# Kernel tuning notes

Hardware: AMD Instinct MI355X
Metric: run time of the kernel (lower is better)

## Reference

```python
import jax, jax.numpy as jnp
import numpy as np

B, P, N, C = 4, 12, 1024, 64  # batch, past window, nodes, channels (in==hidden==out)


def setup_inputs() -> dict:
    key = jax.random.key(0)
    k1, k2, k3, k4, k5, k6 = jax.random.split(key, 6)
    x = jax.random.normal(k1, (B, P, N, C), dtype=jnp.float32)
    # float adjacency mask in {0,1}; force self-loops so no softmax row is empty
    A = jax.random.randint(k2, (B, P, N, N), 0, 2).astype(jnp.float32)
    A = A.at[..., jnp.arange(N), jnp.arange(N)].set(1.0)
    # learned params (nn.Linear stores weight as [out, in]; y = x @ W.T)
    W_emb = jax.random.normal(k3, (C, C), dtype=jnp.float32) / jnp.sqrt(jnp.float32(C))
    a1 = jax.random.normal(k4, (C,), dtype=jnp.float32)
    a2 = jax.random.normal(k5, (C,), dtype=jnp.float32)
    W_lin = jax.random.normal(k6, (C, C), dtype=jnp.float32) / jnp.sqrt(jnp.float32(C))
    return {"x": x, "A": A, "W_emb": W_emb, "a1": a1, "a2": a2, "W_lin": W_lin}


def reference(x, A, W_emb, a1, a2, W_lin):
    # x_emb = emb(x)  (bias-free linear)
    x_emb = jnp.einsum('bpnc,hc->bpnh', x, W_emb)            # [B,P,N,H]
    s1 = x_emb @ a1                                           # [B,P,N]
    s2 = x_emb @ a2                                           # [B,P,N]
    # additive GAT scores: a1_i + a2_j, broadcast instead of repeat
    z = jax.nn.leaky_relu(s1[..., :, None] + s2[..., None, :], 0.01)  # [B,P,N,N]
    z = jnp.where(A == 0.0, -jnp.inf, z)
    pi = jax.nn.softmax(z, axis=-1)                           # masked attention
    agg = jnp.einsum('bpij,bpjc->bpic', pi, x)                # weighted aggregation
    out = jax.nn.sigmoid(jnp.einsum('bpic,oc->bpio', agg, W_lin))
    return (out, A)
```

## Files before the change

kernel.cpp:

```cpp
#include <hip/hip_runtime.h>

typedef __attribute__((ext_vector_type(8))) __bf16 bf16x8;
typedef __attribute__((ext_vector_type(4))) float f32x4;

#define N_ 1024
#define C_ 64
#define BP_ 48

static __device__ __forceinline__ unsigned short f2bf(float f) {
    __bf16 b = (__bf16)f;
    return __builtin_bit_cast(unsigned short, b);
}
static __device__ __forceinline__ unsigned int pack2(float a, float b) {
    return (unsigned int)f2bf(a) | ((unsigned int)f2bf(b) << 16);
}

__global__ __launch_bounds__(256) void gat_pre(
    const float* __restrict__ x, const float* __restrict__ Wemb,
    const float* __restrict__ a1, const float* __restrict__ a2,
    float* __restrict__ s1g, float* __restrict__ s2g,
    unsigned short* __restrict__ xT, float* __restrict__ M2part)
{
    __shared__ float xs[64][65];
    __shared__ float vs[2][64];
    const int t = threadIdx.x, l = t & 63, w = t >> 6;
    const int j0 = blockIdx.x * 64;
    const int bp = blockIdx.y;

    if (w == 0) {
        float v1 = 0.f, v2 = 0.f;
        #pragma unroll 8
        for (int h = 0; h < 64; ++h) {
            float we = Wemb[h * 64 + l];
            v1 = fmaf(a1[h], we, v1);
            v2 = fmaf(a2[h], we, v2);
        }
        vs[0][l] = v1; vs[1][l] = v2;
    }
    const float* xb = x + ((size_t)bp * N_ + j0) * C_;
    #pragma unroll
    for (int it = 0; it < 16; ++it)
        xs[it * 4 + w][l] = xb[(it * 4 + w) * C_ + l];
    __syncthreads();

    const int jr = t >> 2, c0 = (t & 3) * 16;
    float p1 = 0.f, p2 = 0.f;
    #pragma unroll
    for (int k = 0; k < 16; ++k) {
        float xv = xs[jr][c0 + k];
        p1 = fmaf(xv, vs[0][c0 + k], p1);
        p2 = fmaf(xv, vs[1][c0 + k], p2);
    }
    p1 += __shfl_xor(p1, 1); p1 += __shfl_xor(p1, 2);
    p2 += __shfl_xor(p2, 1); p2 += __shfl_xor(p2, 2);
    if ((l & 3) == 0) {
        s1g[bp * N_ + j0 + jr] = p1;
        s2g[bp * N_ + j0 + jr] = p2;
    }
    float m = p2;
    m = fmaxf(m, __shfl_xor(m, 4));
    m = fmaxf(m, __shfl_xor(m, 8));
    m = fmaxf(m, __shfl_xor(m, 16));
    m = fmaxf(m, __shfl_xor(m, 32));
    if (l == 0) M2part[bp * 64 + blockIdx.x * 4 + w] = m;

    const int c = t >> 2, part = t & 3;
    unsigned int ow[8];
    #pragma unroll
    for (int k = 0; k < 16; k += 2) {
        unsigned int lo = f2bf(xs[part * 16 + k][c]);
        unsigned int hi = f2bf(xs[part * 16 + k + 1][c]);
        ow[k >> 1] = lo | (hi << 16);
    }
    uint4* dst = (uint4*)(xT + (size_t)bp * C_ * N_ + (size_t)c * N_ + j0 + part * 16);
    dst[0] = make_uint4(ow[0], ow[1], ow[2], ow[3]);
    dst[1] = make_uint4(ow[4], ow[5], ow[6], ow[7]);
}

__global__ __launch_bounds__(256, 4) void gat_fused(
    const float* __restrict__ Ag, float* __restrict__ outA,
    const unsigned short* __restrict__ xT,
    const float* __restrict__ s1g, const float* __restrict__ s2g,
    const float* __restrict__ M2part,
    const float* __restrict__ Wlin, float* __restrict__ out)
{
    __shared__ unsigned short Plds[4][16][72];
    __shared__ float s2lds[1024];
    __shared__ float lsLDS[4][16];

    const int t = threadIdx.x, l = t & 63, w = t >> 6;
    const int i15 = l & 15, q = l >> 4;
    const int lm = l & 15, g16 = l >> 4;
    const int bp = blockIdx.y;
    const int ibase = blockIdx.x * 64 + w * 16;

    *(f32x4*)&s2lds[4 * t] = *(const f32x4*)&s2g[bp * N_ + 4 * t];

    float m2v = M2part[bp * 64 + l];
    #pragma unroll
    for (int off = 32; off >= 1; off >>= 1)
        m2v = fmaxf(m2v, __shfl_xor(m2v, off));
    const float M2 = m2v;
    const float s1_l = s1g[bp * N_ + ibase + i15];

    float s1r[4], mvr[4];
    #pragma unroll
    for (int sr = 0; sr < 4; ++sr) {
        s1r[sr] = __shfl(s1_l, 4 * sr + g16);
        float zr = s1r[sr] + M2;
        mvr[sr] = fmaxf(zr, 0.01f * zr);
    }

    __syncthreads();

    const float* Arow = Ag + ((size_t)bp * N_ + ibase + g16) * N_ + 4 * lm;
    float* oArow = outA + ((size_t)bp * N_ + ibase + g16) * N_ + 4 * lm;
    const unsigned short* xTb = xT + (size_t)bp * C_ * N_;

    f32x4 acc[4] = {};
    float ls4[4] = {0.f, 0.f, 0.f, 0.f};

    f32x4 Aa0, Aa1, Aa2, Aa3, Ab0, Ab1, Ab2, Ab3;

#define LOADA(d0, d1, d2, d3, kk) do {                                        \
    const float* _p = Arow + (kk) * 64;                                       \
    d0 = *(const f32x4*)(_p);                                                 \
    d1 = *(const f32x4*)(_p + 4 * N_);                                        \
    d2 = *(const f32x4*)(_p + 8 * N_);                                        \
    d3 = *(const f32x4*)(_p + 12 * N_); } while (0)

#define DOSR(Av, sr, j0c) do {                                                \
    *(f32x4*)(oArow + (sr) * 4 * N_ + (j0c)) = Av;                            \
    float e0, e1, e2, e3;                                                     \
    { float zz = s1r[sr] + s2v[0]; zz = fmaxf(zz, 0.01f * zz);                \
      e0 = (Av[0] != 0.f) ? __expf(zz - mvr[sr]) : 0.f; }                     \
    { float zz = s1r[sr] + s2v[1]; zz = fmaxf(zz, 0.01f * zz);                \
      e1 = (Av[1] != 0.f) ? __expf(zz - mvr[sr]) : 0.f; }                     \
    { float zz = s1r[sr] + s2v[2]; zz = fmaxf(zz, 0.01f * zz);                \
      e2 = (Av[2] != 0.f) ? __expf(zz - mvr[sr]) : 0.f; }                     \
    { float zz = s1r[sr] + s2v[3]; zz = fmaxf(zz, 0.01f * zz);                \
      e3 = (Av[3] != 0.f) ? __expf(zz - mvr[sr]) : 0.f; }                     \
    ls4[sr] += (e0 + e1) + (e2 + e3);                                         \
    *(uint2*)&Plds[w][4 * (sr) + g16][4 * lm] =                               \
        make_uint2(pack2(e0, e1), pack2(e2, e3)); } while (0)

#define CONSUME(a0, a1, a2, a3, kk) do {                                      \
    const int j0c = (kk) * 64;                                                \
    const f32x4 s2v = *(const f32x4*)&s2lds[j0c + 4 * lm];                    \
    DOSR(a0, 0, j0c); DOSR(a1, 1, j0c); DOSR(a2, 2, j0c); DOSR(a3, 3, j0c);  \
    _Pragma("unroll")                                                         \
    for (int s = 0; s < 2; ++s) {                                             \
        bf16x8 af = *(const bf16x8*)&Plds[w][i15][s * 32 + q * 8];            \
        _Pragma("unroll")                                                     \
        for (int nt = 0; nt < 4; ++nt) {                                      \
            bf16x8 bfr = *(const bf16x8*)&xTb[(size_t)(nt * 16 + i15) * N_ +  \
                                              j0c + s * 32 + q * 8];          \
            acc[nt] = __builtin_amdgcn_mfma_f32_16x16x32_bf16(af, bfr,        \
                                                              acc[nt], 0, 0, 0); \
        }                                                                     \
    } } while (0)

    LOADA(Aa0, Aa1, Aa2, Aa3, 0);
    #pragma unroll 1
    for (int k = 0; k < 16; k += 2) {
        LOADA(Ab0, Ab1, Ab2, Ab3, k + 1);
        CONSUME(Aa0, Aa1, Aa2, Aa3, k);
        if (k + 2 < 16)
            LOADA(Aa0, Aa1, Aa2, Aa3, k + 2);
        CONSUME(Ab0, Ab1, Ab2, Ab3, k + 1);
    }
#undef LOADA
#undef DOSR
#undef CONSUME

    #pragma unroll
    for (int sr = 0; sr < 4; ++sr) {
        ls4[sr] += __shfl_xor(ls4[sr], 1);
        ls4[sr] += __shfl_xor(ls4[sr], 2);
        ls4[sr] += __shfl_xor(ls4[sr], 4);
        ls4[sr] += __shfl_xor(ls4[sr], 8);
    }
    if (lm == 0) {
        #pragma unroll
        for (int sr = 0; sr < 4; ++sr)
            lsLDS[w][4 * sr + g16] = ls4[sr];
    }
    const f32x4 lsq = *(const f32x4*)&lsLDS[w][4 * q];

    unsigned short* aggl = &Plds[w][0][0];
    #pragma unroll
    for (int nt = 0; nt < 4; ++nt)
        #pragma unroll
        for (int r = 0; r < 4; ++r)
            aggl[(q * 4 + r) * 72 + nt * 16 + i15] = f2bf(acc[nt][r] / lsq[r]);

    f32x4 d2[4] = {};
    #pragma unroll
    for (int s = 0; s < 2; ++s) {
        bf16x8 af = *(const bf16x8*)&aggl[i15 * 72 + s * 32 + q * 8];
        #pragma unroll
        for (int nt = 0; nt < 4; ++nt) {
            const float* wp = Wlin + (size_t)(nt * 16 + i15) * C_ + s * 32 + q * 8;
            f32x4 w0 = *(const f32x4*)wp;
            f32x4 w1 = *(const f32x4*)(wp + 4);
            bf16x8 bfr;
            #pragma unroll
            for (int jj = 0; jj < 4; ++jj) { bfr[jj] = (__bf16)w0[jj]; bfr[4 + jj] = (__bf16)w1[jj]; }
            d2[nt] = __builtin_amdgcn_mfma_f32_16x16x32_bf16(af, bfr, d2[nt], 0, 0, 0);
        }
    }
    float* orow = out + ((size_t)bp * N_ + ibase) * C_;
    #pragma unroll
    for (int nt = 0; nt < 4; ++nt)
        #pragma unroll
        for (int r = 0; r < 4; ++r)
            orow[(size_t)(q * 4 + r) * C_ + nt * 16 + i15] =
                1.f / (1.f + __expf(-d2[nt][r]));
}

extern "C" void kernel_launch(void* const* d_in, const int* in_sizes, int n_in,
                              void* d_out, int out_size, void* d_ws, size_t ws_size,
                              hipStream_t stream) {
    const float* x    = (const float*)d_in[0];
    const float* Ag   = (const float*)d_in[1];
    const float* Wemb = (const float*)d_in[2];
    const float* a1   = (const float*)d_in[3];
    const float* a2   = (const float*)d_in[4];
    const float* Wlin = (const float*)d_in[5];
    float* out  = (float*)d_out;
    float* outA = out + (size_t)BP_ * N_ * C_;

    float* s1g = (float*)d_ws;
    float* s2g = s1g + BP_ * N_;
    float* M2part = s2g + BP_ * N_;
    unsigned short* xT = (unsigned short*)(M2part + BP_ * 64);

    gat_pre<<<dim3(16, BP_), dim3(256), 0, stream>>>(x, Wemb, a1, a2,
                                                     s1g, s2g, xT, M2part);
    gat_fused<<<dim3(16, BP_), dim3(256), 0, stream>>>(Ag, outA, xT, s1g, s2g,
                                                       M2part, Wlin, out);
}
```

Baseline: 403.5 us.

## Split key dimension across wave pairs and double grid for more parallelism

Each block now covers 32 query rows instead of 64. Two waves share each 16-row group, and each of the two handles half of the 1024 key columns. The partial aggregation accumulators and row sums are combined through shared memory before the projection epilogue. The grid doubles to 32x48 blocks and launch bounds rise to 6 blocks per SM, aiming to expose more memory-level parallelism for streaming the large A tensor. In exchange it adds an extra LDS buffer, a block-wide barrier, and idle waves during the epilogue.

```diff
diff --git a/kernel.cpp b/kernel.cpp
--- a/kernel.cpp
+++ b/kernel.cpp
@@ -77,7 +77,7 @@
     dst[1] = make_uint4(ow[4], ow[5], ow[6], ow[7]);
 }
 
-__global__ __launch_bounds__(256, 4) void gat_fused(
+__global__ __launch_bounds__(256, 6) void gat_fused(
     const float* __restrict__ Ag, float* __restrict__ outA,
     const unsigned short* __restrict__ xT,
     const float* __restrict__ s1g, const float* __restrict__ s2g,
@@ -87,12 +87,15 @@
     __shared__ unsigned short Plds[4][16][72];
     __shared__ float s2lds[1024];
     __shared__ float lsLDS[4][16];
+    __shared__ float comb[2][16][68];
 
     const int t = threadIdx.x, l = t & 63, w = t >> 6;
     const int i15 = l & 15, q = l >> 4;
     const int lm = l & 15, g16 = l >> 4;
     const int bp = blockIdx.y;
-    const int ibase = blockIdx.x * 64 + w * 16;
+    const int rg = w >> 1, jh = w & 1;
+    const int ibase = blockIdx.x * 32 + rg * 16;
+    const int jbase = jh * 512;
 
     *(f32x4*)&s2lds[4 * t] = *(const f32x4*)&s2g[bp * N_ + 4 * t];
 
@@ -113,8 +116,8 @@
 
     __syncthreads();
 
-    const float* Arow = Ag + ((size_t)bp * N_ + ibase + g16) * N_ + 4 * lm;
-    float* oArow = outA + ((size_t)bp * N_ + ibase + g16) * N_ + 4 * lm;
+    const float* Arow = Ag + ((size_t)bp * N_ + ibase + g16) * N_ + jbase + 4 * lm;
+    float* oArow = outA + ((size_t)bp * N_ + ibase + g16) * N_ + jbase + 4 * lm;
     const unsigned short* xTb = xT + (size_t)bp * C_ * N_;
 
     f32x4 acc[4] = {};
@@ -129,8 +132,8 @@
     d2 = *(const f32x4*)(_p + 8 * N_);                                        \
     d3 = *(const f32x4*)(_p + 12 * N_); } while (0)
 
-#define DOSR(Av, sr, j0c) do {                                                \
-    *(f32x4*)(oArow + (sr) * 4 * N_ + (j0c)) = Av;                            \
+#define DOSR(Av, sr, jrel) do {                                               \
+    *(f32x4*)(oArow + (sr) * 4 * N_ + (jrel)) = Av;                           \
     float e0, e1, e2, e3;                                                     \
     { float zz = s1r[sr] + s2v[0]; zz = fmaxf(zz, 0.01f * zz);                \
       e0 = (Av[0] != 0.f) ? __expf(zz - mvr[sr]) : 0.f; }                     \
@@ -145,9 +148,10 @@
         make_uint2(pack2(e0, e1), pack2(e2, e3)); } while (0)
 
 #define CONSUME(a0, a1, a2, a3, kk) do {                                      \
-    const int j0c = (kk) * 64;                                                \
+    const int jrel = (kk) * 64;                                               \
+    const int j0c = jbase + jrel;                                             \
     const f32x4 s2v = *(const f32x4*)&s2lds[j0c + 4 * lm];                    \
-    DOSR(a0, 0, j0c); DOSR(a1, 1, j0c); DOSR(a2, 2, j0c); DOSR(a3, 3, j0c);  \
+    DOSR(a0, 0, jrel); DOSR(a1, 1, jrel); DOSR(a2, 2, jrel); DOSR(a3, 3, jrel); \
     _Pragma("unroll")                                                         \
     for (int s = 0; s < 2; ++s) {                                             \
         bf16x8 af = *(const bf16x8*)&Plds[w][i15][s * 32 + q * 8];            \
@@ -162,10 +166,10 @@
 
     LOADA(Aa0, Aa1, Aa2, Aa3, 0);
     #pragma unroll 1
-    for (int k = 0; k < 16; k += 2) {
+    for (int k = 0; k < 8; k += 2) {
         LOADA(Ab0, Ab1, Ab2, Ab3, k + 1);
         CONSUME(Aa0, Aa1, Aa2, Aa3, k);
-        if (k + 2 < 16)
+        if (k + 2 < 8)
             LOADA(Aa0, Aa1, Aa2, Aa3, k + 2);
         CONSUME(Ab0, Ab1, Ab2, Ab3, k + 1);
     }
@@ -185,7 +189,26 @@
         for (int sr = 0; sr < 4; ++sr)
             lsLDS[w][4 * sr + g16] = ls4[sr];
     }
-    const f32x4 lsq = *(const f32x4*)&lsLDS[w][4 * q];
+    if (jh == 1) {
+        #pragma unroll
+        for (int nt = 0; nt < 4; ++nt)
+            #pragma unroll
+            for (int r = 0; r < 4; ++r)
+                comb[rg][q * 4 + r][nt * 16 + i15] = acc[nt][r];
+    }
+    __syncthreads();
+    if (jh == 1) return;
+
+    #pragma unroll
+    for (int nt = 0; nt < 4; ++nt)
+        #pragma unroll
+        for (int r = 0; r < 4; ++r)
+            acc[nt][r] += comb[rg][q * 4 + r][nt * 16 + i15];
+    const f32x4 ls_a = *(const f32x4*)&lsLDS[w][4 * q];
+    const f32x4 ls_b = *(const f32x4*)&lsLDS[w + 1][4 * q];
+    f32x4 lsq;
+    #pragma unroll
+    for (int r = 0; r < 4; ++r) lsq[r] = ls_a[r] + ls_b[r];
 
     unsigned short* aggl = &Plds[w][0][0];
     #pragma unroll
@@ -237,6 +260,6 @@
 
     gat_pre<<<dim3(16, BP_), dim3(256), 0, stream>>>(x, Wemb, a1, a2,
                                                      s1g, s2g, xT, M2part);
-    gat_fused<<<dim3(16, BP_), dim3(256), 0, stream>>>(Ag, outA, xT, s1g, s2g,
+    gat_fused<<<dim3(32, BP_), dim3(256), 0, stream>>>(Ag, outA, xT, s1g, s2g,
                                                        M2part, Wlin, out);
 }
```

Measured after the change: 472.1 us. 1.17x slower.

## Prefetch xT MFMA operands into registers and use nontemporal A load/store

Applied to the files above, without the earlier changes.

The bf16 xT fragments for each 64-column chunk are now loaded into registers one chunk ahead, double-buffered alongside the A tile, so the MFMA B operands are no longer fetched from global memory right before use. A loads and outA stores become nontemporal to avoid polluting cache with the streamed adjacency. Occupancy is lowered to 3 waves-per-SIMD blocks to make room for the extra prefetch registers. The cost is more register pressure and less latency hiding through occupancy.

```diff
diff --git a/kernel.cpp b/kernel.cpp
--- a/kernel.cpp
+++ b/kernel.cpp
@@ -77,7 +77,7 @@
     dst[1] = make_uint4(ow[4], ow[5], ow[6], ow[7]);
 }
 
-__global__ __launch_bounds__(256, 4) void gat_fused(
+__global__ __launch_bounds__(256, 3) void gat_fused(
     const float* __restrict__ Ag, float* __restrict__ outA,
     const unsigned short* __restrict__ xT,
     const float* __restrict__ s1g, const float* __restrict__ s2g,
@@ -115,22 +115,32 @@
 
     const float* Arow = Ag + ((size_t)bp * N_ + ibase + g16) * N_ + 4 * lm;
     float* oArow = outA + ((size_t)bp * N_ + ibase + g16) * N_ + 4 * lm;
-    const unsigned short* xTb = xT + (size_t)bp * C_ * N_;
+    const unsigned short* xTrow = xT + (size_t)bp * C_ * N_ + (size_t)i15 * N_ + q * 8;
 
     f32x4 acc[4] = {};
     float ls4[4] = {0.f, 0.f, 0.f, 0.f};
 
-    f32x4 Aa0, Aa1, Aa2, Aa3, Ab0, Ab1, Ab2, Ab3;
-
-#define LOADA(d0, d1, d2, d3, kk) do {                                        \
+    f32x4 Aa[4], Ab[4];
+    bf16x8 Xa[8], Xb[8];
+
+#define LOADX(X, kk) do {                                                     \
+    _Pragma("unroll")                                                         \
+    for (int nt = 0; nt < 4; ++nt)                                            \
+        _Pragma("unroll")                                                     \
+        for (int s = 0; s < 2; ++s)                                           \
+            X[s * 4 + nt] = *(const bf16x8*)&xTrow[(size_t)nt * 16 * N_ +     \
+                                                   (kk) * 64 + s * 32];       \
+    } while (0)
+
+#define LOADA(Ax, kk) do {                                                    \
     const float* _p = Arow + (kk) * 64;                                       \
-    d0 = *(const f32x4*)(_p);                                                 \
-    d1 = *(const f32x4*)(_p + 4 * N_);                                        \
-    d2 = *(const f32x4*)(_p + 8 * N_);                                        \
-    d3 = *(const f32x4*)(_p + 12 * N_); } while (0)
-
-#define DOSR(Av, sr, j0c) do {                                                \
-    *(f32x4*)(oArow + (sr) * 4 * N_ + (j0c)) = Av;                            \
+    _Pragma("unroll")                                                         \
+    for (int r = 0; r < 4; ++r)                                               \
+        Ax[r] = __builtin_nontemporal_load((const f32x4*)(_p + r * 4 * N_));  \
+    } while (0)
+
+#define DOSR(Av, sr, jrel) do {                                               \
+    __builtin_nontemporal_store(Av, (f32x4*)(oArow + (sr) * 4 * N_ + (jrel)));\
     float e0, e1, e2, e3;                                                     \
     { float zz = s1r[sr] + s2v[0]; zz = fmaxf(zz, 0.01f * zz);                \
       e0 = (Av[0] != 0.f) ? __expf(zz - mvr[sr]) : 0.f; }                     \
@@ -144,31 +154,29 @@
     *(uint2*)&Plds[w][4 * (sr) + g16][4 * lm] =                               \
         make_uint2(pack2(e0, e1), pack2(e2, e3)); } while (0)
 
-#define CONSUME(a0, a1, a2, a3, kk) do {                                      \
-    const int j0c = (kk) * 64;                                                \
-    const f32x4 s2v = *(const f32x4*)&s2lds[j0c + 4 * lm];                    \
-    DOSR(a0, 0, j0c); DOSR(a1, 1, j0c); DOSR(a2, 2, j0c); DOSR(a3, 3, j0c);  \
+#define CONSUME(X, Ac, kk) do {                                               \
+    const int jrel = (kk) * 64;                                               \
+    const f32x4 s2v = *(const f32x4*)&s2lds[jrel + 4 * lm];                   \
+    DOSR(Ac[0], 0, jrel); DOSR(Ac[1], 1, jrel);                               \
+    DOSR(Ac[2], 2, jrel); DOSR(Ac[3], 3, jrel);                               \
     _Pragma("unroll")                                                         \
     for (int s = 0; s < 2; ++s) {                                             \
         bf16x8 af = *(const bf16x8*)&Plds[w][i15][s * 32 + q * 8];            \
         _Pragma("unroll")                                                     \
-        for (int nt = 0; nt < 4; ++nt) {                                      \
-            bf16x8 bfr = *(const bf16x8*)&xTb[(size_t)(nt * 16 + i15) * N_ +  \
-                                              j0c + s * 32 + q * 8];          \
-            acc[nt] = __builtin_amdgcn_mfma_f32_16x16x32_bf16(af, bfr,        \
+        for (int nt = 0; nt < 4; ++nt)                                        \
+            acc[nt] = __builtin_amdgcn_mfma_f32_16x16x32_bf16(af, X[s * 4 + nt], \
                                                               acc[nt], 0, 0, 0); \
-        }                                                                     \
     } } while (0)
 
-    LOADA(Aa0, Aa1, Aa2, Aa3, 0);
+    LOADX(Xa, 0); LOADA(Aa, 0);
     #pragma unroll 1
     for (int k = 0; k < 16; k += 2) {
-        LOADA(Ab0, Ab1, Ab2, Ab3, k + 1);
-        CONSUME(Aa0, Aa1, Aa2, Aa3, k);
-        if (k + 2 < 16)
-            LOADA(Aa0, Aa1, Aa2, Aa3, k + 2);
-        CONSUME(Ab0, Ab1, Ab2, Ab3, k + 1);
-    }
+        LOADX(Xb, k + 1); LOADA(Ab, k + 1);
+        CONSUME(Xa, Aa, k);
+        if (k + 2 < 16) { LOADX(Xa, k + 2); LOADA(Aa, k + 2); }
+        CONSUME(Xb, Ab, k + 1);
+    }
+#undef LOADX
 #undef LOADA
 #undef DOSR
 #undef CONSUME
```

Result: faster. 387.9 us (-3.9%).
